# Optimization experiments

Hardware: AMD Instinct MI355X
Metric: run time of the kernel (lower is better)

Reference implementation:

```python
import jax, jax.numpy as jnp
import numpy as np

N_QUBITS = 12
R = 1
EDGES = [(i, (i + 1) % N_QUBITS) for i in range(N_QUBITS)]
DIM = 2 ** N_QUBITS
BATCH = 64
_LET = 'abcdefghijklmnopqrstuvwxy'

_I4 = np.eye(4, dtype=np.float32)
_AD = np.fliplr(_I4).copy()                      # antidiagonal (XX imag pattern)
_YP = np.array([[0,0,0,1],[0,0,-1,0],[0,-1,0,0],[1,0,0,0]], dtype=np.float32)  # YY imag pattern
_CNOT = jnp.asarray(np.array([[1,0,0,0],[0,1,0,0],[0,0,0,1],[0,0,1,0]], dtype=np.complex64))
_k = np.arange(DIM)
# z_signs[i, k] = -1 if bit (n-i-1) of k is set, matching the torch buffer
_ZS = jnp.asarray(np.stack([1.0 - 2.0 * ((_k >> (N_QUBITS - i - 1)) & 1) for i in range(N_QUBITS)]).astype(np.float32))  # [n, 2^n]


def _c(r, i):
    return jax.lax.complex(r, i)


def rx_mat(t):
    c, s, z = jnp.cos(t / 2), jnp.sin(t / 2), jnp.zeros_like(t)
    real = jnp.stack([jnp.stack([c, z], -1), jnp.stack([z, c], -1)], -2)
    imag = jnp.stack([jnp.stack([z, -s], -1), jnp.stack([-s, z], -1)], -2)
    return _c(real, imag)


def ry_mat(t):
    c, s = jnp.cos(t / 2), jnp.sin(t / 2)
    real = jnp.stack([jnp.stack([c, -s], -1), jnp.stack([s, c], -1)], -2)
    return _c(real, jnp.zeros_like(real))


def rz_mat(t):
    p, z = t / 2, jnp.zeros_like(t)
    cp, sp = jnp.cos(p), jnp.sin(p)
    real = jnp.stack([jnp.stack([cp, z], -1), jnp.stack([z, cp], -1)], -2)
    imag = jnp.stack([jnp.stack([-sp, z], -1), jnp.stack([z, sp], -1)], -2)
    return _c(real, imag)


def ising_zz(t):
    p = t / 2
    c, s = jnp.cos(p), jnp.sin(p)
    dr = jnp.stack([c, c, c, c], -1)
    di = jnp.stack([-s, s, s, -s], -1)
    i4 = jnp.asarray(_I4)
    return _c(dr[..., :, None] * i4, di[..., :, None] * i4)


def ising_xx(t):
    c, s = jnp.cos(t / 2), jnp.sin(t / 2)
    return _c(c[..., None, None] * jnp.asarray(_I4), -s[..., None, None] * jnp.asarray(_AD))


def ising_yy(t):
    c, s = jnp.cos(t / 2), jnp.sin(t / 2)
    return _c(c[..., None, None] * jnp.asarray(_I4), s[..., None, None] * jnp.asarray(_YP))


def apply_1q(state, gate, q):
    # state [B, 2^n]; gate [2,2] or [B,2,2]; qubit axis sits at stride 2^q (matches torch view)
    B = state.shape[0]
    left, right = 2 ** (N_QUBITS - q - 1), 2 ** q
    s = state.reshape(B, left, 2, right)
    sub = 'bij' if gate.ndim == 3 else 'ij'
    return jnp.einsum(f'{sub},bljr->blir', gate, s).reshape(B, DIM)


def apply_2q(state, gate, q1, q2):
    # state [B, 2^n]; gate [4,4]; qubit index = tensor-axis index from MSB (matches torch permute path)
    if q1 > q2:
        q1, q2 = q2, q1
    B = state.shape[0]
    s = state.reshape((B,) + (2,) * N_QUBITS)
    g = gate.reshape(2, 2, 2, 2)
    ax = list(_LET[:N_QUBITS])
    out = ax.copy()
    u, v = ax[q1], ax[q2]
    out[q1], out[q2] = 'A', 'B'
    spec = f"AB{u}{v},Z{''.join(ax)}->Z{''.join(out)}"
    return jnp.einsum(spec, g, s).reshape(B, DIM)


def _forward(data, encoding_scale, encoding_bias, eta, ew_zz, ew_xx, ew_yy, nb_z, nb_x, nb_y, trainable_rots):
    B, n = data.shape
    # data-encoding gates, cached once per forward: angles [B, n] -> gates [B, n, 2, 2]
    rx_g = rx_mat(encoding_scale[:, 0] * data + encoding_bias[:, 0])
    ry_g = ry_mat(encoding_scale[:, 1] * data + encoding_bias[:, 1])
    rz_g = rz_mat(encoding_scale[:, 2] * data + encoding_bias[:, 2])
    state = jnp.zeros((B, DIM), jnp.complex64).at[:, 0].set(1.0)
    ising_fns = (ising_zz, ising_xx, ising_yy)
    ews = (ew_zz, ew_xx, ew_yy)
    nbs = (nb_z, nb_x, nb_y)
    bias_fns = (rz_mat, rx_mat, ry_mat)
    enc_types = ('full', 'xy', 'yz')
    for r in range(R):
        for b in range(3):  # blocks: ZZ, XX, YY
            bt = enc_types[b]
            # data encoding
            for q in range(n):
                if bt != 'yz':
                    state = apply_1q(state, rx_g[:, q], q)
                state = apply_1q(state, ry_g[:, q], q)
                if bt != 'xy':
                    state = apply_1q(state, rz_g[:, q], q)
            # Ising interaction on each edge
            theta = eta[r, b] * ews[b][r]            # [n_edges]
            egs = ising_fns[b](theta)                # [n_edges, 4, 4]
            for e, (i, j) in enumerate(EDGES):
                state = apply_2q(state, egs[e], i, j)
            # node biases (RZ / RX / RY matching the block)
            bgs = bias_fns[b](nbs[b][r])             # [n, 2, 2]
            for q in range(n):
                state = apply_1q(state, bgs[q], q)
            # trainable rotations rx, ry, rz per qubit
            rots = trainable_rots[r, b]              # [n, 3]
            rxg, ryg, rzg = rx_mat(rots[:, 0]), ry_mat(rots[:, 1]), rz_mat(rots[:, 2])
            for q in range(n):
                state = apply_1q(state, rxg[q], q)
                state = apply_1q(state, ryg[q], q)
                state = apply_1q(state, rzg[q], q)
            # CNOT entangling ring
            for q in range(n):
                state = apply_2q(state, _CNOT, q, (q + 1) % n)
    probs = state.real ** 2 + state.imag ** 2        # [B, 2^n]
    return probs @ _ZS.T                             # Pauli-Z expectations [B, n]


def setup_inputs() -> dict:
    key = jax.random.key(0)
    ks = jax.random.split(key, 12)
    n, E, f = N_QUBITS, len(EDGES), jnp.float32
    return {
        'data': jax.random.uniform(ks[0], (BATCH, n), f),
        'encoding_scale': jnp.pi * jnp.ones((n, 3), f) + 0.1 * jax.random.normal(ks[1], (n, 3), f),
        'encoding_bias': 0.1 * jax.random.normal(ks[2], (n, 3), f),
        'eta': 0.5 * jnp.ones((R, 3), f),
        'ew_zz': jnp.ones((R, E), f) + 0.1 * jax.random.normal(ks[3], (R, E), f),
        'ew_xx': jnp.ones((R, E), f) + 0.1 * jax.random.normal(ks[4], (R, E), f),
        'ew_yy': jnp.ones((R, E), f) + 0.1 * jax.random.normal(ks[5], (R, E), f),
        'nb_z': 0.1 * jax.random.normal(ks[6], (R, n), f),
        'nb_x': 0.1 * jax.random.normal(ks[7], (R, n), f),
        'nb_y': 0.1 * jax.random.normal(ks[8], (R, n), f),
        'trainable_rots': 0.1 * jax.random.normal(ks[9], (R, 3, n, 3), f),
    }


def reference(data, encoding_scale, encoding_bias, eta, ew_zz, ew_xx, ew_yy, nb_z, nb_x, nb_y, trainable_rots):
    return _forward(data, encoding_scale, encoding_bias, eta, ew_zz, ew_xx, ew_yy, nb_z, nb_x, nb_y, trainable_rots)
```

## Files before the change

kernel.cpp:

```cpp
#include <hip/hip_runtime.h>
#include <math.h>

#define NT 512
#define QDIM 4096

using F2 = float2;

__device__ __forceinline__ F2 cadd(F2 p, F2 q) { return make_float2(p.x + q.x, p.y + q.y); }
__device__ __forceinline__ F2 cmul(F2 p, F2 q) {
    return make_float2(p.x * q.x - p.y * q.y, p.x * q.y + p.y * q.x);
}

struct M2 { F2 a, b, c, d; };

__device__ __forceinline__ M2 mmul(M2 A, M2 B) {
    M2 R;
    R.a = cadd(cmul(A.a, B.a), cmul(A.b, B.c));
    R.b = cadd(cmul(A.a, B.b), cmul(A.b, B.d));
    R.c = cadd(cmul(A.c, B.a), cmul(A.d, B.c));
    R.d = cadd(cmul(A.c, B.b), cmul(A.d, B.d));
    return R;
}

__device__ __forceinline__ M2 mrx(float t) {
    float s, c; sincosf(0.5f * t, &s, &c);
    return { make_float2(c, 0), make_float2(0, -s), make_float2(0, -s), make_float2(c, 0) };
}
__device__ __forceinline__ M2 mry(float t) {
    float s, c; sincosf(0.5f * t, &s, &c);
    return { make_float2(c, 0), make_float2(-s, 0), make_float2(s, 0), make_float2(c, 0) };
}
__device__ __forceinline__ M2 mrz(float t) {
    float s, c; sincosf(0.5f * t, &s, &c);
    return { make_float2(c, -s), make_float2(0, 0), make_float2(0, 0), make_float2(c, s) };
}

#define RSQ2 0.70710678118654752f
__device__ __forceinline__ M2 mH() {
    return { make_float2(RSQ2, 0), make_float2(RSQ2, 0), make_float2(RSQ2, 0), make_float2(-RSQ2, 0) };
}
__device__ __forceinline__ M2 mW() {
    return { make_float2(RSQ2, 0), make_float2(0, RSQ2), make_float2(RSQ2, 0), make_float2(0, -RSQ2) };
}
__device__ __forceinline__ M2 mWd() {
    return { make_float2(RSQ2, 0), make_float2(RSQ2, 0), make_float2(0, -RSQ2), make_float2(0, RSQ2) };
}


template<int Li>
__device__ __forceinline__ int kOf(int t, int j) {
    const int mlo = (1 << (3 * Li)) - 1;
    return (t & mlo) | (j << (3 * Li)) | ((t & ~mlo) << 3);
}
__device__ __forceinline__ int slot0(int k) {
    int j = k & 7, t = k >> 3;
    return j * 512 + (t ^ j);
}

template<int TYPE>
__device__ __forceinline__ void itrip(F2* amp, int l, F2* wb) {
#pragma unroll
    for (int j = 0; j < 8; ++j) wb[j * 64 + (l ^ ((9 * j) & 63))] = amp[j];
    asm volatile("" ::: "memory");
#pragma unroll
    for (int j = 0; j < 8; ++j) {
        int jo, lo;
        if (TYPE == 0) { jo = l & 7;        lo = j | (l & 56); }
        else           { jo = (l >> 3) & 7; lo = (l & 7) | (j << 3); }
        amp[j] = wb[jo * 64 + (lo ^ ((9 * jo) & 63))];
    }
}

__device__ __forceinline__ void btrip(F2* amp, int tid, int l, int wv, F2* b) {
#pragma unroll
    for (int j = 0; j < 8; ++j) b[j * 512 + (tid ^ j)] = amp[j];
    __syncthreads();
#pragma unroll
    for (int j = 0; j < 8; ++j) amp[j] = b[wv * 512 + ((j * 64 + l) ^ wv)];
}

template<int JB>
__device__ __forceinline__ void g1_reg(F2* amp, const F2* g) {
    const int m = 1 << JB;
    F2 m00 = g[0], m01 = g[1], m10 = g[2], m11 = g[3];
#pragma unroll
    for (int j = 0; j < 8; ++j)
        if (!(j & m)) {
            F2 a = amp[j], b = amp[j | m];
            amp[j]     = cadd(cmul(m00, a), cmul(m01, b));
            amp[j | m] = cadd(cmul(m10, a), cmul(m11, b));
        }
}

__device__ __forceinline__ void diag_L3(F2* amp, const float* zh, int tid) {
    float phi0 = 0.f;
#pragma unroll
    for (int e = 3; e <= 10; ++e) {
        int hi = 11 - e, lo = 10 - e;
        phi0 += (((tid >> hi) ^ (tid >> lo)) & 1) ? zh[e] : -zh[e];
    }
    float z0 = zh[0], z1 = zh[1], z2 = zh[2], z11 = zh[11];
    int t8 = (tid >> 8) & 1, t0 = tid & 1;
#pragma unroll
    for (int j = 0; j < 8; ++j) {
        int j0 = j & 1, j1 = (j >> 1) & 1, j2 = (j >> 2) & 1;
        float phi = phi0
            + ((j2 ^ j1) ? z0 : -z0)
            + ((j1 ^ j0) ? z1 : -z1)
            + ((j0 ^ t8) ? z2 : -z2)
            + ((j2 ^ t0) ? z11 : -z11);
        float sp, cp;
        __sincosf(phi, &sp, &cp);
        amp[j] = cmul(amp[j], make_float2(cp, sp));
    }
}

__device__ __forceinline__ int cnot_src(int k) {
#pragma unroll
    for (int e = 11; e >= 0; --e) {
        int hi = (e < 11) ? 11 - e : 11, lo = (e < 11) ? 10 - e : 0;
        if ((k >> hi) & 1) k ^= (1 << lo);
    }
    return k;
}

__device__ __forceinline__ void cnot_trip(F2* amp, int tid, const int* kslot, F2* b) {
#pragma unroll
    for (int j = 0; j < 8; ++j) b[j * 512 + (tid ^ j)] = amp[j];
    __syncthreads();
#pragma unroll
    for (int j = 0; j < 8; ++j) amp[j] = b[kslot[j]];
}

__global__ __launch_bounds__(NT) void qsim_kernel(
    const float* __restrict__ data,
    const float* __restrict__ enc_scale,
    const float* __restrict__ enc_bias,
    const float* __restrict__ eta,
    const float* __restrict__ ew_zz,
    const float* __restrict__ ew_xx,
    const float* __restrict__ ew_yy,
    const float* __restrict__ nb_z,
    const float* __restrict__ nb_x,
    const float* __restrict__ nb_y,
    const float* __restrict__ trots,
    float* __restrict__ out)
{
    __shared__ F2 bbuf[2][QDIM];
    __shared__ F2 ibuf[QDIM];
    __shared__ F2 g1q[72][4];
    __shared__ float zhalf[3][12];
    __shared__ float red[8][12];

    const int tid = threadIdx.x;
    const int l = tid & 63, wv = tid >> 6;
    const int bat = blockIdx.x;
    F2* wb = &ibuf[wv * 512];

    if (tid < 36) {
        int b = tid / 12, q = tid % 12;
        float x  = data[bat * 12 + q];
        float ax = enc_scale[q * 3 + 0] * x + enc_bias[q * 3 + 0];
        float ay = enc_scale[q * 3 + 1] * x + enc_bias[q * 3 + 1];
        float az = enc_scale[q * 3 + 2] * x + enc_bias[q * 3 + 2];
        M2 M;
        if (b == 0)      M = mmul(mrz(az), mmul(mry(ay), mrx(ax)));
        else if (b == 1) M = mmul(mH(), mmul(mry(ay), mrx(ax)));
        else             M = mmul(mW(), mmul(mrz(az), mry(ay)));
        g1q[tid][0] = M.a; g1q[tid][1] = M.b; g1q[tid][2] = M.c; g1q[tid][3] = M.d;
    } else if (tid < 72) {
        int i = tid - 36, b = i / 12, q = i % 12;
        float nb = (b == 0) ? nb_z[q] : (b == 1) ? nb_x[q] : nb_y[q];
        M2 M0 = (b == 0) ? mrz(nb) : (b == 1) ? mrx(nb) : mry(nb);
        float t0 = trots[(b * 12 + q) * 3 + 0];
        float t1 = trots[(b * 12 + q) * 3 + 1];
        float t2 = trots[(b * 12 + q) * 3 + 2];
        M2 M = mmul(mrz(t2), mmul(mry(t1), mmul(mrx(t0), M0)));
        if (b == 1)      M = mmul(M, mH());
        else if (b == 2) M = mmul(M, mWd());
        g1q[tid][0] = M.a; g1q[tid][1] = M.b; g1q[tid][2] = M.c; g1q[tid][3] = M.d;
    } else if (tid < 108) {
        int i = tid - 72, b = i / 12, e = i % 12;
        const float* ew = (b == 0) ? ew_zz : (b == 1) ? ew_xx : ew_yy;
        zhalf[b][e] = 0.5f * eta[b] * ew[e];
    }
    __syncthreads();

    F2 amp[8];
#pragma unroll
    for (int j = 0; j < 8; ++j) amp[j] = make_float2(0.f, 0.f);
    if (tid == 0) amp[0].x = 1.f;

    int kslot[8];
#pragma unroll
    for (int j = 0; j < 8; ++j)
        kslot[j] = slot0(cnot_src(kOf<0>(tid, j)));

    int sel = 0;
#define NB (&bbuf[(sel ^= 1) ^ 1][0])

    for (int blk = 0; blk < 3; ++blk) {
        const F2(*Ge)[4] = &g1q[blk * 12];
        const F2(*Gb)[4] = &g1q[36 + blk * 12];

        g1_reg<0>(amp, Ge[0]);  g1_reg<1>(amp, Ge[1]);  g1_reg<2>(amp, Ge[2]);
        itrip<0>(amp, l, wb);
        g1_reg<0>(amp, Ge[3]);  g1_reg<1>(amp, Ge[4]);  g1_reg<2>(amp, Ge[5]);
        itrip<1>(amp, l, wb);
        g1_reg<0>(amp, Ge[6]);  g1_reg<1>(amp, Ge[7]);  g1_reg<2>(amp, Ge[8]);
        btrip(amp, tid, l, wv, NB);
        g1_reg<0>(amp, Ge[9]);  g1_reg<1>(amp, Ge[10]); g1_reg<2>(amp, Ge[11]);

        diag_L3(amp, zhalf[blk], tid);

        g1_reg<0>(amp, Gb[9]);  g1_reg<1>(amp, Gb[10]); g1_reg<2>(amp, Gb[11]);
        btrip(amp, tid, l, wv, NB);
        g1_reg<0>(amp, Gb[6]);  g1_reg<1>(amp, Gb[7]);  g1_reg<2>(amp, Gb[8]);
        itrip<1>(amp, l, wb);
        g1_reg<0>(amp, Gb[3]);  g1_reg<1>(amp, Gb[4]);  g1_reg<2>(amp, Gb[5]);
        itrip<0>(amp, l, wb);
        g1_reg<0>(amp, Gb[0]);  g1_reg<1>(amp, Gb[1]);  g1_reg<2>(amp, Gb[2]);

        cnot_trip(amp, tid, kslot, NB);
    }

    float pr[8];
#pragma unroll
    for (int j = 0; j < 8; ++j) pr[j] = amp[j].x * amp[j].x + amp[j].y * amp[j].y;
    float psum = 0.f;
#pragma unroll
    for (int j = 0; j < 8; ++j) psum += pr[j];

    float acc[12];
#pragma unroll
    for (int i = 0; i < 9; ++i)
        acc[i] = ((tid >> (8 - i)) & 1) ? -psum : psum;
#pragma unroll
    for (int i = 9; i < 12; ++i) {
        float s = 0.f;
        int bit = 11 - i;
#pragma unroll
        for (int j = 0; j < 8; ++j)
            s += ((j >> bit) & 1) ? -pr[j] : pr[j];
        acc[i] = s;
    }
#pragma unroll
    for (int off = 32; off > 0; off >>= 1)
#pragma unroll
        for (int i = 0; i < 12; ++i)
            acc[i] += __shfl_down(acc[i], off, 64);
    if ((tid & 63) == 0)
#pragma unroll
        for (int i = 0; i < 12; ++i) red[wv][i] = acc[i];
    __syncthreads();
    if (tid < 12) {
        float s = 0.f;
#pragma unroll
        for (int ww = 0; ww < 8; ++ww) s += red[ww][tid];
        out[bat * 12 + tid] = s;
    }
}

extern "C" void kernel_launch(void* const* d_in, const int* in_sizes, int n_in,
                              void* d_out, int out_size, void* d_ws, size_t ws_size,
                              hipStream_t stream) {
    const float* data      = (const float*)d_in[0];
    const float* enc_scale = (const float*)d_in[1];
    const float* enc_bias  = (const float*)d_in[2];
    const float* eta       = (const float*)d_in[3];
    const float* ew_zz     = (const float*)d_in[4];
    const float* ew_xx     = (const float*)d_in[5];
    const float* ew_yy     = (const float*)d_in[6];
    const float* nb_z      = (const float*)d_in[7];
    const float* nb_x      = (const float*)d_in[8];
    const float* nb_y      = (const float*)d_in[9];
    const float* trots     = (const float*)d_in[10];
    float* out = (float*)d_out;

    int batch = out_size / 12;
    qsim_kernel<<<batch, NT, 0, stream>>>(data, enc_scale, enc_bias, eta,
                                          ew_zz, ew_xx, ew_yy,
                                          nb_z, nb_x, nb_y, trots, out);
}
```

Before: 100.3 us.

## Move gate-matrix precompute into a separate prep kernel reading via global/scalar loads

```diff
diff --git a/kernel.cpp b/kernel.cpp
--- a/kernel.cpp
+++ b/kernel.cpp
@@ -3,6 +3,7 @@
 
 #define NT 512
 #define QDIM 4096
+#define GT_STRIDE 640
 
 using F2 = float2;
 
@@ -46,6 +47,49 @@
     return { make_float2(RSQ2, 0), make_float2(RSQ2, 0), make_float2(0, -RSQ2), make_float2(0, RSQ2) };
 }
 
+__global__ __launch_bounds__(128) void prep_kernel(
+    const float* __restrict__ data, const float* __restrict__ enc_scale,
+    const float* __restrict__ enc_bias, const float* __restrict__ eta,
+    const float* __restrict__ ew_zz, const float* __restrict__ ew_xx,
+    const float* __restrict__ ew_yy, const float* __restrict__ nb_z,
+    const float* __restrict__ nb_x, const float* __restrict__ nb_y,
+    const float* __restrict__ trots, float* __restrict__ gt)
+{
+    const int bat = blockIdx.x, tid = threadIdx.x;
+    float* g = gt + bat * GT_STRIDE;
+    if (tid < 36) {
+        int b = tid / 12, q = tid % 12;
+        float x  = data[bat * 12 + q];
+        float ax = enc_scale[q * 3 + 0] * x + enc_bias[q * 3 + 0];
+        float ay = enc_scale[q * 3 + 1] * x + enc_bias[q * 3 + 1];
+        float az = enc_scale[q * 3 + 2] * x + enc_bias[q * 3 + 2];
+        M2 M;
+        if (b == 0)      M = mmul(mrz(az), mmul(mry(ay), mrx(ax)));
+        else if (b == 1) M = mmul(mH(), mmul(mry(ay), mrx(ax)));
+        else             M = mmul(mW(), mmul(mrz(az), mry(ay)));
+        float* o = g + tid * 8;
+        o[0] = M.a.x; o[1] = M.a.y; o[2] = M.b.x; o[3] = M.b.y;
+        o[4] = M.c.x; o[5] = M.c.y; o[6] = M.d.x; o[7] = M.d.y;
+    } else if (tid < 72) {
+        int i = tid - 36, b = i / 12, q = i % 12;
+        float nb = (b == 0) ? nb_z[q] : (b == 1) ? nb_x[q] : nb_y[q];
+        M2 M0 = (b == 0) ? mrz(nb) : (b == 1) ? mrx(nb) : mry(nb);
+        float t0 = trots[(b * 12 + q) * 3 + 0];
+        float t1 = trots[(b * 12 + q) * 3 + 1];
+        float t2 = trots[(b * 12 + q) * 3 + 2];
+        M2 M = mmul(mrz(t2), mmul(mry(t1), mmul(mrx(t0), M0)));
+        if (b == 1)      M = mmul(M, mH());
+        else if (b == 2) M = mmul(M, mWd());
+        float* o = g + tid * 8;
+        o[0] = M.a.x; o[1] = M.a.y; o[2] = M.b.x; o[3] = M.b.y;
+        o[4] = M.c.x; o[5] = M.c.y; o[6] = M.d.x; o[7] = M.d.y;
+    } else if (tid < 108) {
+        int i = tid - 72, b = i / 12, e = i % 12;
+        const float* ew = (b == 0) ? ew_zz : (b == 1) ? ew_xx : ew_yy;
+        g[576 + i] = 0.5f * eta[b] * ew[e];
+    }
+}
+
 
 template<int Li>
 __device__ __forceinline__ int kOf(int t, int j) {
@@ -80,9 +124,10 @@
 }
 
 template<int JB>
-__device__ __forceinline__ void g1_reg(F2* amp, const F2* g) {
+__device__ __forceinline__ void g1_reg(F2* amp, const float* __restrict__ g) {
     const int m = 1 << JB;
-    F2 m00 = g[0], m01 = g[1], m10 = g[2], m11 = g[3];
+    F2 m00 = make_float2(g[0], g[1]), m01 = make_float2(g[2], g[3]);
+    F2 m10 = make_float2(g[4], g[5]), m11 = make_float2(g[6], g[7]);
 #pragma unroll
     for (int j = 0; j < 8; ++j)
         if (!(j & m)) {
@@ -92,7 +137,7 @@
         }
 }
 
-__device__ __forceinline__ void diag_L3(F2* amp, const float* zh, int tid) {
+__device__ __forceinline__ void diag_L3(F2* amp, const float* __restrict__ zh, int tid) {
     float phi0 = 0.f;
 #pragma unroll
     for (int e = 3; e <= 10; ++e) {
@@ -133,58 +178,18 @@
 }
 
 __global__ __launch_bounds__(NT) void qsim_kernel(
-    const float* __restrict__ data,
-    const float* __restrict__ enc_scale,
-    const float* __restrict__ enc_bias,
-    const float* __restrict__ eta,
-    const float* __restrict__ ew_zz,
-    const float* __restrict__ ew_xx,
-    const float* __restrict__ ew_yy,
-    const float* __restrict__ nb_z,
-    const float* __restrict__ nb_x,
-    const float* __restrict__ nb_y,
-    const float* __restrict__ trots,
+    const float* __restrict__ gt,
     float* __restrict__ out)
 {
     __shared__ F2 bbuf[2][QDIM];
     __shared__ F2 ibuf[QDIM];
-    __shared__ F2 g1q[72][4];
-    __shared__ float zhalf[3][12];
     __shared__ float red[8][12];
 
     const int tid = threadIdx.x;
     const int l = tid & 63, wv = tid >> 6;
     const int bat = blockIdx.x;
     F2* wb = &ibuf[wv * 512];
-
-    if (tid < 36) {
-        int b = tid / 12, q = tid % 12;
-        float x  = data[bat * 12 + q];
-        float ax = enc_scale[q * 3 + 0] * x + enc_bias[q * 3 + 0];
-        float ay = enc_scale[q * 3 + 1] * x + enc_bias[q * 3 + 1];
-        float az = enc_scale[q * 3 + 2] * x + enc_bias[q * 3 + 2];
-        M2 M;
-        if (b == 0)      M = mmul(mrz(az), mmul(mry(ay), mrx(ax)));
-        else if (b == 1) M = mmul(mH(), mmul(mry(ay), mrx(ax)));
-        else             M = mmul(mW(), mmul(mrz(az), mry(ay)));
-        g1q[tid][0] = M.a; g1q[tid][1] = M.b; g1q[tid][2] = M.c; g1q[tid][3] = M.d;
-    } else if (tid < 72) {
-        int i = tid - 36, b = i / 12, q = i % 12;
-        float nb = (b == 0) ? nb_z[q] : (b == 1) ? nb_x[q] : nb_y[q];
-        M2 M0 = (b == 0) ? mrz(nb) : (b == 1) ? mrx(nb) : mry(nb);
-        float t0 = trots[(b * 12 + q) * 3 + 0];
-        float t1 = trots[(b * 12 + q) * 3 + 1];
-        float t2 = trots[(b * 12 + q) * 3 + 2];
-        M2 M = mmul(mrz(t2), mmul(mry(t1), mmul(mrx(t0), M0)));
-        if (b == 1)      M = mmul(M, mH());
-        else if (b == 2) M = mmul(M, mWd());
-        g1q[tid][0] = M.a; g1q[tid][1] = M.b; g1q[tid][2] = M.c; g1q[tid][3] = M.d;
-    } else if (tid < 108) {
-        int i = tid - 72, b = i / 12, e = i % 12;
-        const float* ew = (b == 0) ? ew_zz : (b == 1) ? ew_xx : ew_yy;
-        zhalf[b][e] = 0.5f * eta[b] * ew[e];
-    }
-    __syncthreads();
+    const float* __restrict__ G = gt + bat * GT_STRIDE;
 
     F2 amp[8];
 #pragma unroll
@@ -200,26 +205,27 @@
 #define NB (&bbuf[(sel ^= 1) ^ 1][0])
 
     for (int blk = 0; blk < 3; ++blk) {
-        const F2(*Ge)[4] = &g1q[blk * 12];
-        const F2(*Gb)[4] = &g1q[36 + blk * 12];
-
-        g1_reg<0>(amp, Ge[0]);  g1_reg<1>(amp, Ge[1]);  g1_reg<2>(amp, Ge[2]);
+        const float* Ge = G + blk * 96;
+        const float* Gb = G + 288 + blk * 96;
+        const float* zh = G + 576 + blk * 12;
+
+        g1_reg<0>(amp, Ge + 0);   g1_reg<1>(amp, Ge + 8);   g1_reg<2>(amp, Ge + 16);
         itrip<0>(amp, l, wb);
-        g1_reg<0>(amp, Ge[3]);  g1_reg<1>(amp, Ge[4]);  g1_reg<2>(amp, Ge[5]);
+        g1_reg<0>(amp, Ge + 24);  g1_reg<1>(amp, Ge + 32);  g1_reg<2>(amp, Ge + 40);
         itrip<1>(amp, l, wb);
-        g1_reg<0>(amp, Ge[6]);  g1_reg<1>(amp, Ge[7]);  g1_reg<2>(amp, Ge[8]);
+        g1_reg<0>(amp, Ge + 48);  g1_reg<1>(amp, Ge + 56);  g1_reg<2>(amp, Ge + 64);
         btrip(amp, tid, l, wv, NB);
-        g1_reg<0>(amp, Ge[9]);  g1_reg<1>(amp, Ge[10]); g1_reg<2>(amp, Ge[11]);
-
-        diag_L3(amp, zhalf[blk], tid);
-
-        g1_reg<0>(amp, Gb[9]);  g1_reg<1>(amp, Gb[10]); g1_reg<2>(amp, Gb[11]);
+        g1_reg<0>(amp, Ge + 72);  g1_reg<1>(amp, Ge + 80);  g1_reg<2>(amp, Ge + 88);
+
+        diag_L3(amp, zh, tid);
+
+        g1_reg<0>(amp, Gb + 72);  g1_reg<1>(amp, Gb + 80);  g1_reg<2>(amp, Gb + 88);
         btrip(amp, tid, l, wv, NB);
-        g1_reg<0>(amp, Gb[6]);  g1_reg<1>(amp, Gb[7]);  g1_reg<2>(amp, Gb[8]);
+        g1_reg<0>(amp, Gb + 48);  g1_reg<1>(amp, Gb + 56);  g1_reg<2>(amp, Gb + 64);
         itrip<1>(amp, l, wb);
-        g1_reg<0>(amp, Gb[3]);  g1_reg<1>(amp, Gb[4]);  g1_reg<2>(amp, Gb[5]);
+        g1_reg<0>(amp, Gb + 24);  g1_reg<1>(amp, Gb + 32);  g1_reg<2>(amp, Gb + 40);
         itrip<0>(amp, l, wb);
-        g1_reg<0>(amp, Gb[0]);  g1_reg<1>(amp, Gb[1]);  g1_reg<2>(amp, Gb[2]);
+        g1_reg<0>(amp, Gb + 0);   g1_reg<1>(amp, Gb + 8);   g1_reg<2>(amp, Gb + 16);
 
         cnot_trip(amp, tid, kslot, NB);
     }
@@ -276,9 +282,11 @@
     const float* nb_y      = (const float*)d_in[9];
     const float* trots     = (const float*)d_in[10];
     float* out = (float*)d_out;
+    float* gt  = (float*)d_ws;
 
     int batch = out_size / 12;
-    qsim_kernel<<<batch, NT, 0, stream>>>(data, enc_scale, enc_bias, eta,
-                                          ew_zz, ew_xx, ew_yy,
-                                          nb_z, nb_x, nb_y, trots, out);
-}
+    prep_kernel<<<batch, 128, 0, stream>>>(data, enc_scale, enc_bias, eta,
+                                           ew_zz, ew_xx, ew_yy,
+                                           nb_z, nb_x, nb_y, trots, gt);
+    qsim_kernel<<<batch, NT, 0, stream>>>(gt, out);
+}
```

After: 101.3 us. About the same (+1.0%).
